# Optimization experiments

Hardware: AMD Instinct MI355X
Metric: run time of the kernel (lower is better)

## Reference

```python
import jax, jax.numpy as jnp
import numpy as np

K = 9          # kernel_size
CENTER = K // 2
EXTEND = 1.0   # extend_scope
B, C_IN, C_OUT, H, W = 2, 64, 64, 256, 256


def group_norm(x, w, b, groups, eps=1e-5):
    Bx, C, Hx, Wx = x.shape
    xg = x.reshape(Bx, groups, C // groups, Hx, Wx)
    m = xg.mean(axis=(2, 3, 4), keepdims=True)
    v = xg.var(axis=(2, 3, 4), keepdims=True)
    xn = ((xg - m) * jax.lax.rsqrt(v + eps)).reshape(Bx, C, Hx, Wx)
    return xn * w[None, :, None, None] + b[None, :, None, None]


def conv2d(x, w, b, stride, padding):
    y = jax.lax.conv_general_dilated(x, w, stride, padding,
                                     dimension_numbers=('NCHW', 'OIHW', 'NCHW'))
    return y + b[None, :, None, None]


def bilinear_sample(feat, iy, ix):
    # feat [B,C,H,W]; iy/ix pixel coords [B,Hg,Wg]; align_corners=True bilinear
    Hf, Wf = feat.shape[2], feat.shape[3]
    y0 = jnp.floor(iy); x0 = jnp.floor(ix)
    wy1 = iy - y0; wx1 = ix - x0
    wy0 = 1.0 - wy1; wx0 = 1.0 - wx1
    y0i = jnp.clip(y0, 0, Hf - 1).astype(jnp.int32)
    y1i = jnp.clip(y0 + 1, 0, Hf - 1).astype(jnp.int32)
    x0i = jnp.clip(x0, 0, Wf - 1).astype(jnp.int32)
    x1i = jnp.clip(x0 + 1, 0, Wf - 1).astype(jnp.int32)
    g = jax.vmap(lambda f, yi, xi: f[:, yi, xi])  # per-batch gather -> [B,C,Hg,Wg]
    return (g(feat, y0i, x0i) * (wy0 * wx0)[:, None]
            + g(feat, y0i, x1i) * (wy0 * wx1)[:, None]
            + g(feat, y1i, x0i) * (wy1 * wx0)[:, None]
            + g(feat, y1i, x1i) * (wy1 * wx1)[:, None])


def outward_cumsum(off):
    # off [B,K,H,W]: center row -> 0, cumulative sums outward from center
    lower = jnp.flip(jnp.cumsum(jnp.flip(off[:, :CENTER], axis=1), axis=1), axis=1)
    upper = jnp.cumsum(off[:, CENTER + 1:], axis=1)
    zero = jnp.zeros_like(off[:, :1])
    return jnp.concatenate([lower, zero, upper], axis=1)


def reference(x, w_off, b_off, gno_w, gno_b, w_dsc, b_dsc, gn_w, gn_b):
    Bx, _, Hx, Wx = x.shape
    # offset branch: conv3x3 -> GroupNorm(K, 2K) -> tanh
    offset = conv2d(x, w_off, b_off, (1, 1), ((1, 1), (1, 1)))
    offset = jnp.tanh(group_norm(offset, gno_w, gno_b, groups=K))
    y_off = offset[:, :K]                      # morph=0 uses the y half
    y_cum = outward_cumsum(y_off)              # [B,K,H,W]
    y_center = jnp.arange(Hx, dtype=x.dtype)[None, None, :, None]
    x_base = (jnp.arange(Wx, dtype=x.dtype)[None, None, None, :]
              + jnp.linspace(-CENTER, CENTER, K, dtype=x.dtype)[None, :, None, None])
    y_new = y_center + EXTEND * y_cum          # [B,K,H,W]
    x_new = jnp.broadcast_to(x_base, y_new.shape)
    # permute(0,2,1,3).reshape -> [B, K*H, W]
    ycoord = y_new.transpose(0, 2, 1, 3).reshape(Bx, Hx * K, Wx)
    xcoord = x_new.transpose(0, 2, 1, 3).reshape(Bx, Hx * K, Wx)
    # clamp to [0,max] then [-1,1] normalize + align_corners unnormalize == clamp
    iy = jnp.clip(ycoord, 0.0, Hx - 1.0)
    ix = jnp.clip(xcoord, 0.0, Wx - 1.0)
    deformed = bilinear_sample(x, iy, ix)      # [B,C,K*H,W]
    out = conv2d(deformed, w_dsc, b_dsc, (K, 1), 'VALID')  # [B,Cout,H,W]
    out = group_norm(out, gn_w, gn_b, groups=C_OUT // 4)
    return jax.nn.relu(out)


def setup_inputs() -> dict:
    key = jax.random.key(0)
    ks = jax.random.split(key, 3)
    return {
        'x': jax.random.normal(ks[0], (B, C_IN, H, W), dtype=jnp.float32),
        'w_off': jax.random.normal(ks[1], (2 * K, C_IN, 3, 3), dtype=jnp.float32) * 0.05,
        'b_off': jnp.zeros((2 * K,), dtype=jnp.float32),
        'gno_w': jnp.ones((2 * K,), dtype=jnp.float32),
        'gno_b': jnp.zeros((2 * K,), dtype=jnp.float32),
        'w_dsc': jax.random.normal(ks[2], (C_OUT, C_IN, K, 1), dtype=jnp.float32) * 0.05,
        'b_dsc': jnp.zeros((C_OUT,), dtype=jnp.float32),
        'gn_w': jnp.ones((C_OUT,), dtype=jnp.float32),
        'gn_b': jnp.zeros((C_OUT,), dtype=jnp.float32),
    }
```

## Files before the change

kernel.cpp:

```cpp
#include <hip/hip_runtime.h>
#include <hip/hip_fp16.h>
#include <math.h>

#define BB 2
#define CC 64
#define HH 256
#define WW 256
#define KK 9
#define NOFF 10
#define HW (HH*WW)

typedef __attribute__((ext_vector_type(8))) short s16x8;
typedef __attribute__((ext_vector_type(4))) float f32x4;

__device__ __forceinline__ unsigned lerp2h(unsigned a, unsigned b, __half2 fy2) {
    __half2 ah = *(__half2*)&a, bh = *(__half2*)&b;
    __half2 d = __hfma2(fy2, __hsub2(bh, ah), ah);
    return *(unsigned*)&d;
}

__device__ __forceinline__ float fast_tanh(float z) {
    float e = __builtin_amdgcn_exp2f(z * 2.885390081777927f);
    return 1.f - 2.f * __builtin_amdgcn_rcpf(e + 1.f);
}

__device__ __forceinline__ void swizzle_bhw(int g, int& b, int& h, int& wt) {
    int W = ((g & 7) << 8) | (g >> 3);
    b  = W >> 10;
    int rem = W & 1023;
    h  = rem >> 2;
    wt = rem & 3;
}

__global__ __launch_bounds__(256) void transpose_x_kernel(const float* __restrict__ x,
                                                          unsigned short* __restrict__ xTh,
                                                          const float* __restrict__ w_off,
                                                          const float* __restrict__ w_dsc,
                                                          unsigned short* __restrict__ woffB,
                                                          unsigned short* __restrict__ wdscB) {
    if (blockIdx.x >= 2048) {
        int idx = (blockIdx.x - 2048) * 256 + threadIdx.x;
        if (idx < 18 * 64 * 8) {
            int kb = idx >> 9;
            int L  = (idx >> 3) & 63;
            int j  = idx & 7;
            int n = L & 15, quad = L >> 4;
            int kk = kb * 32 + quad * 8 + j;
            int tap = kk >> 6, ci = kk & 63;
            float v = (n < NOFF) ? w_off[(n * 64 + ci) * 9 + tap] : 0.f;
            __half hv = __float2half(v);
            woffB[idx] = *(unsigned short*)&hv;
        }
        if (idx < 4 * 18 * 64 * 8) {
            int nt = idx / 9216;
            int r  = idx - nt * 9216;
            int kb = r >> 9;
            int L  = (r >> 3) & 63;
            int j  = r & 7;
            int n = L & 15, quad = L >> 4;
            int co = nt * 16 + n;
            int kk = kb * 32 + quad * 8 + j;
            int k = kk >> 6, ci = kk & 63;
            __half hv = __float2half(w_dsc[(co * 64 + ci) * 9 + k]);
            wdscB[idx] = *(unsigned short*)&hv;
        }
        return;
    }
    __shared__ float tile[64 * 65];
    int wt = blockIdx.x & 3;
    int h  = (blockIdx.x >> 2) & 255;
    int b  = blockIdx.x >> 10;
    int w0 = wt * 64;
    int t  = threadIdx.x;
    {
        int wq = t & 15, c0 = t >> 4;
#pragma unroll
        for (int it = 0; it < 4; ++it) {
            int c = c0 + it * 16;
            float4 v = *(const float4*)&x[(((b * CC + c) * HH + h) * WW) + w0 + wq * 4];
            tile[(wq * 4 + 0) * 65 + c] = v.x;
            tile[(wq * 4 + 1) * 65 + c] = v.y;
            tile[(wq * 4 + 2) * 65 + c] = v.z;
            tile[(wq * 4 + 3) * 65 + c] = v.w;
        }
    }
    __syncthreads();
    {
        int c8 = t & 7, wr = t >> 3;
        uint4* dst = (uint4*)xTh;
#pragma unroll
        for (int it = 0; it < 2; ++it) {
            int wl = wr + it * 32;
            const float* row = &tile[wl * 65 + c8 * 8];
            __half2 p0 = __floats2half2_rn(row[0], row[1]);
            __half2 p1 = __floats2half2_rn(row[2], row[3]);
            __half2 p2 = __floats2half2_rn(row[4], row[5]);
            __half2 p3 = __floats2half2_rn(row[6], row[7]);
            uint4 d;
            d.x = *(unsigned*)&p0; d.y = *(unsigned*)&p1;
            d.z = *(unsigned*)&p2; d.w = *(unsigned*)&p3;
            dst[((size_t)((b * HH + h) * WW) + w0 + wl) * 8 + c8] = d;
        }
    }
}

#define CPITCH 72
__global__ __launch_bounds__(256, 4) void conv_off_mfma(const unsigned short* __restrict__ xTh,
                                                        const unsigned short* __restrict__ woffB,
                                                        const float* __restrict__ b_off,
                                                        unsigned short* __restrict__ off_raw,
                                                        float* __restrict__ partials_off) {
    __shared__ unsigned short sx[3 * 66 * CPITCH];
    __shared__ float rs[4][16], rs2[4][16];
    int t = threadIdx.x;
    int L = t & 63, v = t >> 6;
    int b, h, wt;
    swizzle_bhw(blockIdx.x, b, h, wt);
    int w0 = wt << 6;
    int col = L & 15, quad = L >> 4;

#pragma unroll
    for (int it = 0; it < 7; ++it) {
        int linear = it * 256 + t;
        if (linear < 1584) {
            int dy  = linear / 528;
            int rem = linear - dy * 528;
            int px  = rem >> 3, cg = rem & 7;
            int y  = h - 1 + dy;
            int xc = w0 - 1 + px;
            uint4 d = make_uint4(0, 0, 0, 0);
            if ((unsigned)y < 256u && (unsigned)xc < 256u)
                d = *(const uint4*)(xTh + ((size_t)(((b << 8) + y) << 8) + xc) * 64 + cg * 8);
            *(uint4*)&sx[(dy * 66 + px) * CPITCH + cg * 8] = d;
        }
    }

    s16x8 breg[18];
#pragma unroll
    for (int kb = 0; kb < 18; ++kb)
        breg[kb] = *(const s16x8*)(woffB + (kb * 64 + L) * 8);
    __syncthreads();

    f32x4 acc = {0.f, 0.f, 0.f, 0.f};
    __builtin_amdgcn_s_setprio(1);
#pragma unroll
    for (int kb = 0; kb < 18; ++kb) {
        int tap = kb >> 1;
        int dy = tap / 3, dxl = tap % 3;
        int pxl = v * 16 + col + dxl;
        int ci0 = ((kb & 1) << 5) + quad * 8;
        s16x8 a = *(const s16x8*)&sx[(dy * 66 + pxl) * CPITCH + ci0];
        acc = __builtin_amdgcn_mfma_f32_16x16x32_f16(a, breg[kb], acc, 0, 0, 0);
    }
    __builtin_amdgcn_s_setprio(0);
    int oc = col;
    float bo = b_off[oc];
    float s = 0.f, s2 = 0.f;
#pragma unroll
    for (int r = 0; r < 4; ++r) {
        float val = acc[r] + bo;
        if (oc < NOFF) {
            int w = w0 + v * 16 + quad * 4 + r;
            __half hv = __float2half(val);
            off_raw[((b * NOFF + oc) << 16) + (h << 8) + w] = *(unsigned short*)&hv;
        }
        s += val; s2 += val * val;
    }
    s  += __shfl_xor(s, 16, 64);  s  += __shfl_xor(s, 32, 64);
    s2 += __shfl_xor(s2, 16, 64); s2 += __shfl_xor(s2, 32, 64);
    if (quad == 0) { rs[v][oc] = s; rs2[v][oc] = s2; }
    __syncthreads();
    if (t < NOFF) {
        float a_ = rs[0][t] + rs[1][t] + rs[2][t] + rs[3][t];
        float a2 = rs2[0][t] + rs2[1][t] + rs2[2][t] + rs2[3][t];
        partials_off[(size_t)blockIdx.x * 20 + t * 2]     = a_;
        partials_off[(size_t)blockIdx.x * 20 + t * 2 + 1] = a2;
    }
}

__global__ __launch_bounds__(256) void reduce_off_kernel(const float* __restrict__ partials,
                                                         float* __restrict__ stats) {
    int bg = blockIdx.x;
    int t = threadIdx.x;
    float s = 0.f, s2 = 0.f;
    int b = bg / 5, gg = bg - b * 5;
    for (int i = t; i < 2048; i += 256) {
        int blk_b = (((i & 7) << 8) | (i >> 3)) >> 10;
        if (blk_b == b) {
            const float* p = partials + (size_t)i * 20 + gg * 4;
            s  += p[0] + p[2];
            s2 += p[1] + p[3];
        }
    }
    __shared__ float rs[256], rs2[256];
    rs[t] = s; rs2[t] = s2;
    __syncthreads();
    for (int o = 128; o > 0; o >>= 1) {
        if (t < o) { rs[t] += rs[t + o]; rs2[t] += rs2[t + o]; }
        __syncthreads();
    }
    if (t == 0) {
        float mean = rs[0] * (1.f / 131072.f);
        float var  = rs2[0] * (1.f / 131072.f) - mean * mean;
        stats[bg * 2]     = mean;
        stats[bg * 2 + 1] = rsqrtf(var + 1e-5f);
    }
}

__global__ __launch_bounds__(256) void reduce_out_kernel(const float* __restrict__ partials,
                                                         float* __restrict__ stats) {
    int bg = blockIdx.x;
    int b = bg >> 4, g = bg & 15;
    int t = threadIdx.x;
    float s = 0.f, s2 = 0.f;
    for (int i = t; i < 2048; i += 256) {
        int blk_b = (((i & 7) << 8) | (i >> 3)) >> 10;
        if (blk_b == b) {
            const float* p = partials + (size_t)i * 32 + g * 2;
            s  += p[0];
            s2 += p[1];
        }
    }
    __shared__ float rs[256], rs2[256];
    rs[t] = s; rs2[t] = s2;
    __syncthreads();
    for (int o = 128; o > 0; o >>= 1) {
        if (t < o) { rs[t] += rs[t + o]; rs2[t] += rs2[t + o]; }
        __syncthreads();
    }
    if (t == 0) {
        float mean = rs[0] * (1.f / 262144.f);
        float var  = rs2[0] * (1.f / 262144.f) - mean * mean;
        stats[bg * 2]     = mean;
        stats[bg * 2 + 1] = rsqrtf(var + 1e-5f);
    }
}

__global__ __launch_bounds__(256, 4) void main_mfma(const unsigned short* __restrict__ xTh,
                                                    const unsigned short* __restrict__ off_raw,
                                                    const float* __restrict__ stats_off,
                                                    const float* __restrict__ gno_w,
                                                    const float* __restrict__ gno_b,
                                                    const unsigned short* __restrict__ wdscB,
                                                    const float* __restrict__ b_dsc,
                                                    unsigned short* __restrict__ tmph,
                                                    float* __restrict__ partials_out) {
    __shared__ unsigned short aT[32 * 584];
    __shared__ unsigned       coordA[576];

    int t = threadIdx.x;
    int L = t & 63, nt = t >> 6;
    int b, h, wt;
    swizzle_bhw(blockIdx.x, b, h, wt);
    int w0 = wt << 6;

    if (t < 64) {
        int w = w0 + t;
        float tk[9];
#pragma unroll
        for (int k = 0; k < 9; ++k) {
            unsigned short u = off_raw[((b * NOFF + k) << 16) + (h << 8) + w];
            float vv = __half2float(*(__half*)&u);
            int g = k >> 1;
            float mean = stats_off[(b * 5 + g) * 2];
            float rstd = stats_off[(b * 5 + g) * 2 + 1];
            tk[k] = fast_tanh((vv - mean) * rstd * gno_w[k] + gno_b[k]);
        }
        float yc[9];
        float c = 0.f;
#pragma unroll
        for (int k = 3; k >= 0; --k) { c += tk[k]; yc[k] = c; }
        yc[4] = 0.f;
        c = 0.f;
#pragma unroll
        for (int k = 5; k < 9; ++k) { c += tk[k]; yc[k] = c; }
#pragma unroll
        for (int k = 0; k < 9; ++k) {
            float y = fminf(fmaxf((float)h + yc[k], 0.f), 255.f);
            float y0f = floorf(y);
            int y0 = (int)y0f;
            int xc = min(max(w + k - 4, 0), 255);
            __half fh = __float2half(y - y0f);
            coordA[t * 9 + k] = (unsigned)y0 | ((unsigned)xc << 8)
                              | ((unsigned)(*(unsigned short*)&fh) << 16);
        }
    }

    s16x8 wreg[18];
#pragma unroll
    for (int kb = 0; kb < 18; ++kb)
        wreg[kb] = *(const s16x8*)(wdscB + ((nt * 18 + kb) * 64 + L) * 8);

    int col = L & 15, quad = L >> 4;
    int co = nt * 16 + col;
    float bias = b_dsc[co];
    float ss = 0.f, ss2 = 0.f;
    int bBase = b << 22;

    for (int round = 0; round < 2; ++round) {
        __syncthreads();
#pragma unroll
        for (int it = 0; it < 9; ++it) {
            int idx = it * 256 + t;
            int cg  = idx & 7;
            int r2  = idx >> 3;
            int pxl = r2 / 9;
            int k   = r2 - pxl * 9;
            int pi  = (round * 32 + pxl) * 9 + k;
            unsigned pc = coordA[pi];
            int o0 = bBase + ((pc & 255) << 14) + (((pc >> 8) & 255) << 6) + cg * 8;
            unsigned short fb = (unsigned short)(pc >> 16);
            int o1 = fb ? o0 + 16384 : o0;
            __half fh = *(__half*)&fb;
            __half2 fy2 = __half2half2(fh);
            uint4 u0 = *(const uint4*)(xTh + o0);
            uint4 u1 = *(const uint4*)(xTh + o1);
            uint4 d;
            d.x = lerp2h(u0.x, u1.x, fy2);
            d.y = lerp2h(u0.y, u1.y, fy2);
            d.z = lerp2h(u0.z, u1.z, fy2);
            d.w = lerp2h(u0.w, u1.w, fy2);
            int c2 = (cg + k) & 7;
            *(uint4*)&aT[pxl * 584 + k * 64 + c2 * 8] = d;
        }
        __syncthreads();

#pragma unroll
        for (int sub = 0; sub < 2; ++sub) {
            int row = sub * 16 + col;
            f32x4 acc = {0.f, 0.f, 0.f, 0.f};
            __builtin_amdgcn_s_setprio(1);
#pragma unroll
            for (int kb = 0; kb < 18; ++kb) {
                int k  = kb >> 1;
                int cch = ((kb & 1) << 2) + quad;
                int c2 = (cch + k) & 7;
                s16x8 a = *(const s16x8*)&aT[row * 584 + k * 64 + c2 * 8];
                acc = __builtin_amdgcn_mfma_f32_16x16x32_f16(a, wreg[kb], acc, 0, 0, 0);
            }
            __builtin_amdgcn_s_setprio(0);
            int wbase = w0 + round * 32 + sub * 16 + quad * 4;
            size_t obase = ((size_t)((b << 16) + (h << 8) + wbase)) * 64 + co;
#pragma unroll
            for (int r = 0; r < 4; ++r) {
                float val = acc[r] + bias;
                ss += val; ss2 += val * val;
                __half hv = __float2half(val);
                tmph[obase + (size_t)r * 64] = *(unsigned short*)&hv;
            }
        }
    }
    ss  += __shfl_xor(ss, 16, 64);  ss  += __shfl_xor(ss, 32, 64);
    ss2 += __shfl_xor(ss2, 16, 64); ss2 += __shfl_xor(ss2, 32, 64);
    float sg = ss, sg2 = ss2;
    sg  += __shfl_xor(sg, 1, 64);  sg  += __shfl_xor(sg, 2, 64);
    sg2 += __shfl_xor(sg2, 1, 64); sg2 += __shfl_xor(sg2, 2, 64);
    if (quad == 0 && (col & 3) == 0) {
        int gi = nt * 4 + (col >> 2);
        partials_out[(size_t)blockIdx.x * 32 + gi * 2]     = sg;
        partials_out[(size_t)blockIdx.x * 32 + gi * 2 + 1] = sg2;
    }
}

__global__ __launch_bounds__(256) void apply_final_kernel(const unsigned short* __restrict__ tmph,
                                                          const float* __restrict__ stats_out,
                                                          const float* __restrict__ gn_w,
                                                          const float* __restrict__ gn_b,
                                                          float* __restrict__ out) {
    __shared__ float tile[64 * 65];
    int wt = blockIdx.x & 3;
    int h  = (blockIdx.x >> 2) & 255;
    int b  = blockIdx.x >> 10;
    int w0 = wt * 64;
    int t  = threadIdx.x;
    {
        int c8 = t & 7, wr = t >> 3;
        int co0 = c8 * 8;
        float sc[8], sh[8];
#pragma unroll
        for (int j = 0; j < 8; ++j) {
            int g = (co0 + j) >> 2;
            float mean = stats_out[(b * 16 + g) * 2];
            float rstd = stats_out[(b * 16 + g) * 2 + 1];
            sc[j] = rstd * gn_w[co0 + j];
            sh[j] = gn_b[co0 + j] - mean * sc[j];
        }
        const uint4* src = (const uint4*)tmph;
#pragma unroll
        for (int it = 0; it < 2; ++it) {
            int wl = wr + it * 32;
            uint4 u = src[((size_t)((b * HH + h) * WW) + w0 + wl) * 8 + c8];
            float2 f0 = __half22float2(*(__half2*)&u.x);
            float2 f1 = __half22float2(*(__half2*)&u.y);
            float2 f2 = __half22float2(*(__half2*)&u.z);
            float2 f3 = __half22float2(*(__half2*)&u.w);
            tile[(co0 + 0) * 65 + wl] = fmaxf(fmaf(f0.x, sc[0], sh[0]), 0.f);
            tile[(co0 + 1) * 65 + wl] = fmaxf(fmaf(f0.y, sc[1], sh[1]), 0.f);
            tile[(co0 + 2) * 65 + wl] = fmaxf(fmaf(f1.x, sc[2], sh[2]), 0.f);
            tile[(co0 + 3) * 65 + wl] = fmaxf(fmaf(f1.y, sc[3], sh[3]), 0.f);
            tile[(co0 + 4) * 65 + wl] = fmaxf(fmaf(f2.x, sc[4], sh[4]), 0.f);
            tile[(co0 + 5) * 65 + wl] = fmaxf(fmaf(f2.y, sc[5], sh[5]), 0.f);
            tile[(co0 + 6) * 65 + wl] = fmaxf(fmaf(f3.x, sc[6], sh[6]), 0.f);
            tile[(co0 + 7) * 65 + wl] = fmaxf(fmaf(f3.y, sc[7], sh[7]), 0.f);
        }
    }
    __syncthreads();
    {
        int wq = t & 15, c0 = t >> 4;
#pragma unroll
        for (int it = 0; it < 4; ++it) {
            int co = c0 + it * 16;
            const float* row = &tile[co * 65 + wq * 4];
            float4 v;
            v.x = row[0]; v.y = row[1]; v.z = row[2]; v.w = row[3];
            *(float4*)&out[((size_t)(b * CC + co) * HH + h) * WW + w0 + wq * 4] = v;
        }
    }
}

extern "C" void kernel_launch(void* const* d_in, const int* in_sizes, int n_in,
                              void* d_out, int out_size, void* d_ws, size_t ws_size,
                              hipStream_t stream) {
    const float* x     = (const float*)d_in[0];
    const float* w_off = (const float*)d_in[1];
    const float* b_off = (const float*)d_in[2];
    const float* gno_w = (const float*)d_in[3];
    const float* gno_b = (const float*)d_in[4];
    const float* w_dsc = (const float*)d_in[5];
    const float* b_dsc = (const float*)d_in[6];
    const float* gn_w  = (const float*)d_in[7];
    const float* gn_b  = (const float*)d_in[8];
    float* out = (float*)d_out;

    char* ws = (char*)d_ws;
    unsigned short* xTh     = (unsigned short*)(ws);
    unsigned short* tmph    = (unsigned short*)(ws + 16777216);
    unsigned short* off_raw = (unsigned short*)(ws + 33554432);
    unsigned short* wdscB   = (unsigned short*)(ws + 36175872);
    unsigned short* woffB   = (unsigned short*)(ws + 36249600);
    float* stats_off        = (float*)(ws + 36268032);
    float* stats_out        = (float*)(ws + 36268288);
    float* partials_off     = (float*)(ws + 36268544);
    float* partials_out     = (float*)(ws + 36432384);

    hipLaunchKernelGGL(transpose_x_kernel, dim3(2192), dim3(256), 0, stream,
                       x, xTh, w_off, w_dsc, woffB, wdscB);
    hipLaunchKernelGGL(conv_off_mfma, dim3(2048), dim3(256), 0, stream,
                       xTh, woffB, b_off, off_raw, partials_off);
    hipLaunchKernelGGL(reduce_off_kernel, dim3(10), dim3(256), 0, stream,
                       partials_off, stats_off);
    hipLaunchKernelGGL(main_mfma, dim3(2048), dim3(256), 0, stream,
                       xTh, off_raw, stats_off, gno_w, gno_b, wdscB, b_dsc,
                       tmph, partials_out);
    hipLaunchKernelGGL(reduce_out_kernel, dim3(32), dim3(256), 0, stream,
                       partials_out, stats_out);
    hipLaunchKernelGGL(apply_final_kernel, dim3(2048), dim3(256), 0, stream,
                       tmph, stats_out, gn_w, gn_b, out);
}
```

Before: 157.9 us.

## Replace GroupNorm partial-reduction kernels with atomic accumulation into global sums

Removes the two small reduction kernels and has conv_off_mfma and main_mfma atomically add their per-block sums and sums of squares into per-(batch,group) accumulators. The accumulators are zeroed in the transpose kernel. Mean and rstd are now computed by the consumer kernels from the raw sums. Separately, main_mfma precomputes the gather base offset plus a separate half fraction in LDS, which cuts index arithmetic in the gather loop. This saves two launches and their serialization, at the cost of atomic contention from about 2048 blocks per reduction and non-deterministic float summation order.

```diff
diff --git a/kernel.cpp b/kernel.cpp
--- a/kernel.cpp
+++ b/kernel.cpp
@@ -37,9 +37,16 @@
                                                           const float* __restrict__ w_off,
                                                           const float* __restrict__ w_dsc,
                                                           unsigned short* __restrict__ woffB,
-                                                          unsigned short* __restrict__ wdscB) {
+                                                          unsigned short* __restrict__ wdscB,
+                                                          float* __restrict__ sums_off,
+                                                          float* __restrict__ sums_out) {
     if (blockIdx.x >= 2048) {
         int idx = (blockIdx.x - 2048) * 256 + threadIdx.x;
+        if (blockIdx.x == 2048) {
+            int t = threadIdx.x;
+            if (t < 20) sums_off[t] = 0.f;
+            if (t < 64) sums_out[t] = 0.f;
+        }
         if (idx < 18 * 64 * 8) {
             int kb = idx >> 9;
             int L  = (idx >> 3) & 63;
@@ -109,7 +116,7 @@
                                                         const unsigned short* __restrict__ woffB,
                                                         const float* __restrict__ b_off,
                                                         unsigned short* __restrict__ off_raw,
-                                                        float* __restrict__ partials_off) {
+                                                        float* __restrict__ sums_off) {
     __shared__ unsigned short sx[3 * 66 * CPITCH];
     __shared__ float rs[4][16], rs2[4][16];
     int t = threadIdx.x;
@@ -173,88 +180,42 @@
     if (t < NOFF) {
         float a_ = rs[0][t] + rs[1][t] + rs[2][t] + rs[3][t];
         float a2 = rs2[0][t] + rs2[1][t] + rs2[2][t] + rs2[3][t];
-        partials_off[(size_t)blockIdx.x * 20 + t * 2]     = a_;
-        partials_off[(size_t)blockIdx.x * 20 + t * 2 + 1] = a2;
-    }
-}
-
-__global__ __launch_bounds__(256) void reduce_off_kernel(const float* __restrict__ partials,
-                                                         float* __restrict__ stats) {
-    int bg = blockIdx.x;
-    int t = threadIdx.x;
-    float s = 0.f, s2 = 0.f;
-    int b = bg / 5, gg = bg - b * 5;
-    for (int i = t; i < 2048; i += 256) {
-        int blk_b = (((i & 7) << 8) | (i >> 3)) >> 10;
-        if (blk_b == b) {
-            const float* p = partials + (size_t)i * 20 + gg * 4;
-            s  += p[0] + p[2];
-            s2 += p[1] + p[3];
-        }
-    }
-    __shared__ float rs[256], rs2[256];
-    rs[t] = s; rs2[t] = s2;
-    __syncthreads();
-    for (int o = 128; o > 0; o >>= 1) {
-        if (t < o) { rs[t] += rs[t + o]; rs2[t] += rs2[t + o]; }
-        __syncthreads();
-    }
-    if (t == 0) {
-        float mean = rs[0] * (1.f / 131072.f);
-        float var  = rs2[0] * (1.f / 131072.f) - mean * mean;
-        stats[bg * 2]     = mean;
-        stats[bg * 2 + 1] = rsqrtf(var + 1e-5f);
-    }
-}
-
-__global__ __launch_bounds__(256) void reduce_out_kernel(const float* __restrict__ partials,
-                                                         float* __restrict__ stats) {
-    int bg = blockIdx.x;
-    int b = bg >> 4, g = bg & 15;
-    int t = threadIdx.x;
-    float s = 0.f, s2 = 0.f;
-    for (int i = t; i < 2048; i += 256) {
-        int blk_b = (((i & 7) << 8) | (i >> 3)) >> 10;
-        if (blk_b == b) {
-            const float* p = partials + (size_t)i * 32 + g * 2;
-            s  += p[0];
-            s2 += p[1];
-        }
-    }
-    __shared__ float rs[256], rs2[256];
-    rs[t] = s; rs2[t] = s2;
-    __syncthreads();
-    for (int o = 128; o > 0; o >>= 1) {
-        if (t < o) { rs[t] += rs[t + o]; rs2[t] += rs2[t + o]; }
-        __syncthreads();
-    }
-    if (t == 0) {
-        float mean = rs[0] * (1.f / 262144.f);
-        float var  = rs2[0] * (1.f / 262144.f) - mean * mean;
-        stats[bg * 2]     = mean;
-        stats[bg * 2 + 1] = rsqrtf(var + 1e-5f);
+        atomicAdd(&sums_off[(b * 5 + (t >> 1)) * 2],     a_);
+        atomicAdd(&sums_off[(b * 5 + (t >> 1)) * 2 + 1], a2);
     }
 }
 
 __global__ __launch_bounds__(256, 4) void main_mfma(const unsigned short* __restrict__ xTh,
                                                     const unsigned short* __restrict__ off_raw,
-                                                    const float* __restrict__ stats_off,
+                                                    const float* __restrict__ sums_off,
                                                     const float* __restrict__ gno_w,
                                                     const float* __restrict__ gno_b,
                                                     const unsigned short* __restrict__ wdscB,
                                                     const float* __restrict__ b_dsc,
                                                     unsigned short* __restrict__ tmph,
-                                                    float* __restrict__ partials_out) {
+                                                    float* __restrict__ sums_out) {
     __shared__ unsigned short aT[32 * 584];
-    __shared__ unsigned       coordA[576];
+    __shared__ unsigned       offs[576];
+    __shared__ unsigned short fys[576];
 
     int t = threadIdx.x;
     int L = t & 63, nt = t >> 6;
     int b, h, wt;
     swizzle_bhw(blockIdx.x, b, h, wt);
     int w0 = wt << 6;
+    int bBase = b << 22;
 
     if (t < 64) {
+        float msg[5], rsg[5];
+#pragma unroll
+        for (int g = 0; g < 5; ++g) {
+            float s0 = sums_off[(b * 5 + g) * 2];
+            float s1 = sums_off[(b * 5 + g) * 2 + 1];
+            float mean = s0 * (1.f / 131072.f);
+            float var  = s1 * (1.f / 131072.f) - mean * mean;
+            msg[g] = mean;
+            rsg[g] = rsqrtf(var + 1e-5f);
+        }
         int w = w0 + t;
         float tk[9];
 #pragma unroll
@@ -262,9 +223,7 @@
             unsigned short u = off_raw[((b * NOFF + k) << 16) + (h << 8) + w];
             float vv = __half2float(*(__half*)&u);
             int g = k >> 1;
-            float mean = stats_off[(b * 5 + g) * 2];
-            float rstd = stats_off[(b * 5 + g) * 2 + 1];
-            tk[k] = fast_tanh((vv - mean) * rstd * gno_w[k] + gno_b[k]);
+            tk[k] = fast_tanh((vv - msg[g]) * rsg[g] * gno_w[k] + gno_b[k]);
         }
         float yc[9];
         float c = 0.f;
@@ -281,8 +240,8 @@
             int y0 = (int)y0f;
             int xc = min(max(w + k - 4, 0), 255);
             __half fh = __float2half(y - y0f);
-            coordA[t * 9 + k] = (unsigned)y0 | ((unsigned)xc << 8)
-                              | ((unsigned)(*(unsigned short*)&fh) << 16);
+            offs[t * 9 + k] = (unsigned)(bBase + (y0 << 14) + (xc << 6));
+            fys[t * 9 + k]  = *(unsigned short*)&fh;
         }
     }
 
@@ -295,7 +254,6 @@
     int co = nt * 16 + col;
     float bias = b_dsc[co];
     float ss = 0.f, ss2 = 0.f;
-    int bBase = b << 22;
 
     for (int round = 0; round < 2; ++round) {
         __syncthreads();
@@ -307,10 +265,9 @@
             int pxl = r2 / 9;
             int k   = r2 - pxl * 9;
             int pi  = (round * 32 + pxl) * 9 + k;
-            unsigned pc = coordA[pi];
-            int o0 = bBase + ((pc & 255) << 14) + (((pc >> 8) & 255) << 6) + cg * 8;
-            unsigned short fb = (unsigned short)(pc >> 16);
-            int o1 = fb ? o0 + 16384 : o0;
+            unsigned o0 = offs[pi] + (cg << 3);
+            unsigned short fb = fys[pi];
+            unsigned o1 = fb ? o0 + 16384 : o0;
             __half fh = *(__half*)&fb;
             __half2 fy2 = __half2half2(fh);
             uint4 u0 = *(const uint4*)(xTh + o0);
@@ -357,13 +314,13 @@
     sg2 += __shfl_xor(sg2, 1, 64); sg2 += __shfl_xor(sg2, 2, 64);
     if (quad == 0 && (col & 3) == 0) {
         int gi = nt * 4 + (col >> 2);
-        partials_out[(size_t)blockIdx.x * 32 + gi * 2]     = sg;
-        partials_out[(size_t)blockIdx.x * 32 + gi * 2 + 1] = sg2;
+        atomicAdd(&sums_out[(b * 16 + gi) * 2],     sg);
+        atomicAdd(&sums_out[(b * 16 + gi) * 2 + 1], sg2);
     }
 }
 
 __global__ __launch_bounds__(256) void apply_final_kernel(const unsigned short* __restrict__ tmph,
-                                                          const float* __restrict__ stats_out,
+                                                          const float* __restrict__ sums_out,
                                                           const float* __restrict__ gn_w,
                                                           const float* __restrict__ gn_b,
                                                           float* __restrict__ out) {
@@ -376,14 +333,23 @@
     {
         int c8 = t & 7, wr = t >> 3;
         int co0 = c8 * 8;
+        int g0 = co0 >> 2;
+        float meanv[2], rstdv[2];
+#pragma unroll
+        for (int gg = 0; gg < 2; ++gg) {
+            float s0 = sums_out[(b * 16 + g0 + gg) * 2];
+            float s1 = sums_out[(b * 16 + g0 + gg) * 2 + 1];
+            float mean = s0 * (1.f / 262144.f);
+            float var  = s1 * (1.f / 262144.f) - mean * mean;
+            meanv[gg] = mean;
+            rstdv[gg] = rsqrtf(var + 1e-5f);
+        }
         float sc[8], sh[8];
 #pragma unroll
         for (int j = 0; j < 8; ++j) {
-            int g = (co0 + j) >> 2;
-            float mean = stats_out[(b * 16 + g) * 2];
-            float rstd = stats_out[(b * 16 + g) * 2 + 1];
-            sc[j] = rstd * gn_w[co0 + j];
-            sh[j] = gn_b[co0 + j] - mean * sc[j];
+            int gg = j >> 2;
+            sc[j] = rstdv[gg] * gn_w[co0 + j];
+            sh[j] = gn_b[co0 + j] - meanv[gg] * sc[j];
         }
         const uint4* src = (const uint4*)tmph;
 #pragma unroll
@@ -438,22 +404,16 @@
     unsigned short* off_raw = (unsigned short*)(ws + 33554432);
     unsigned short* wdscB   = (unsigned short*)(ws + 36175872);
     unsigned short* woffB   = (unsigned short*)(ws + 36249600);
-    float* stats_off        = (float*)(ws + 36268032);
-    float* stats_out        = (float*)(ws + 36268288);
-    float* partials_off     = (float*)(ws + 36268544);
-    float* partials_out     = (float*)(ws + 36432384);
+    float* sums_off         = (float*)(ws + 36268032);
+    float* sums_out         = (float*)(ws + 36268288);
 
     hipLaunchKernelGGL(transpose_x_kernel, dim3(2192), dim3(256), 0, stream,
-                       x, xTh, w_off, w_dsc, woffB, wdscB);
+                       x, xTh, w_off, w_dsc, woffB, wdscB, sums_off, sums_out);
     hipLaunchKernelGGL(conv_off_mfma, dim3(2048), dim3(256), 0, stream,
-                       xTh, woffB, b_off, off_raw, partials_off);
-    hipLaunchKernelGGL(reduce_off_kernel, dim3(10), dim3(256), 0, stream,
-                       partials_off, stats_off);
+                       xTh, woffB, b_off, off_raw, sums_off);
     hipLaunchKernelGGL(main_mfma, dim3(2048), dim3(256), 0, stream,
-                       xTh, off_raw, stats_off, gno_w, gno_b, wdscB, b_dsc,
-                       tmph, partials_out);
-    hipLaunchKernelGGL(reduce_out_kernel, dim3(32), dim3(256), 0, stream,
-                       partials_out, stats_out);
+                       xTh, off_raw, sums_off, gno_w, gno_b, wdscB, b_dsc,
+                       tmph, sums_out);
     hipLaunchKernelGGL(apply_final_kernel, dim3(2048), dim3(256), 0, stream,
-                       tmph, stats_out, gn_w, gn_b, out);
-}
+                       tmph, sums_out, gn_w, gn_b, out);
+}
```

Result: slower. 410.8 us (+160.2%).
